# Performance work log

Hardware: AMD Instinct MI355X
Metric: run time of the kernel (lower is better)

## Reference

```python
import jax, jax.numpy as jnp
import numpy as np

VAR0, VAR1 = 0.1, 0.2      # cfg['variance']
THR = 0.5                   # overlap_thresh
NEGPOS_RATIO = 3


def point_form(p):  # center form [P,4] -> corner form
    return jnp.concatenate([p[:, :2] - p[:, 2:] / 2, p[:, :2] + p[:, 2:] / 2], axis=1)


def iou(a, b):  # a [N,4], b [P,4], both corner form -> [N,P]
    lt = jnp.maximum(a[:, None, :2], b[None, :, :2])
    rb = jnp.minimum(a[:, None, 2:], b[None, :, 2:])
    wh = jnp.maximum(rb - lt, 0.0)
    inter = wh[..., 0] * wh[..., 1]
    area_a = (a[:, 2] - a[:, 0]) * (a[:, 3] - a[:, 1])
    area_b = (b[:, 2] - b[:, 0]) * (b[:, 3] - b[:, 1])
    return inter / (area_a[:, None] + area_b[None, :] - inter)


def encode(matched, priors):  # matched corner [P,4], priors center [P,4]
    g_cxcy = ((matched[:, :2] + matched[:, 2:]) / 2 - priors[:, :2]) / (VAR0 * priors[:, 2:])
    g_wh = jnp.log((matched[:, 2:] - matched[:, :2]) / priors[:, 2:]) / VAR1
    return jnp.concatenate([g_cxcy, g_wh], axis=1)


def match_one(truths, labels, priors):
    # truths [N,4] corner, labels [N] int, priors [P,4] center
    ov = iou(truths, point_form(priors))            # [N,P]
    best_prior_idx = jnp.argmax(ov, axis=1)         # [N] best prior per truth
    best_truth_overlap = jnp.max(ov, axis=0)        # [P]
    best_truth_idx = jnp.argmax(ov, axis=0)         # [P]
    # ensure every truth keeps its best prior
    best_truth_overlap = best_truth_overlap.at[best_prior_idx].set(2.0)
    best_truth_idx = best_truth_idx.at[best_prior_idx].set(jnp.arange(truths.shape[0]))
    matched = truths[best_truth_idx]                # [P,4]
    conf = jnp.where(best_truth_overlap < THR, 0, labels[best_truth_idx] + 1)  # bkg=0
    return encode(matched, priors), conf


def multibox_loss(loc_data, conf_data, priors, truths, labels):
    B, P, C = conf_data.shape
    loc_t, conf_t = jax.vmap(lambda t, l: match_one(t, l, priors))(truths, labels)
    loc_t = jax.lax.stop_gradient(loc_t)            # targets are detached
    pos = conf_t > 0                                # [B,P]

    # localization: masked smooth-L1 (beta=1), sum reduction
    d = loc_data - loc_t
    ad = jnp.abs(d)
    sl1 = jnp.where(ad < 1.0, 0.5 * d * d, ad - 0.5)
    loss_l = jnp.sum(sl1 * pos[..., None].astype(sl1.dtype))

    # hard negative mining: per-prior CE proxy, positives zeroed, double argsort rank
    lse = jax.nn.logsumexp(conf_data, axis=2)
    gathered = jnp.take_along_axis(conf_data, conf_t[..., None], axis=2)[..., 0]
    lc = jnp.where(pos, 0.0, lse - gathered)        # [B,P]
    loss_idx = jnp.argsort(-lc, axis=1)
    idx_rank = jnp.argsort(loss_idx, axis=1)
    num_pos = jnp.sum(pos, axis=1)                  # [B]
    num_neg = jnp.minimum(NEGPOS_RATIO * num_pos, P - 1)
    neg = idx_rank < num_neg[:, None]
    sel = pos | neg

    # confidence loss on pos + hard negatives, sum reduction
    logp = jax.nn.log_softmax(conf_data, axis=2)
    ce = -jnp.take_along_axis(logp, conf_t[..., None], axis=2)[..., 0]
    loss_c = jnp.sum(ce * sel.astype(ce.dtype))

    total = jnp.sum(num_pos).astype(loss_l.dtype)
    return loss_l / total, loss_c / total


def setup_inputs() -> dict:
    key = jax.random.key(0)
    kl, kc, kp, kt, ky = jax.random.split(key, 5)
    B, P, C, N = 64, 24564, 21, 16
    loc_data = 0.1 * jax.random.normal(kl, (B, P, 4), dtype=jnp.float32)
    conf_data = jax.random.normal(kc, (B, P, C), dtype=jnp.float32)
    pr = jax.random.uniform(kp, (P, 4), dtype=jnp.float32)
    priors = jnp.concatenate([pr[:, :2] * 0.9 + 0.05, pr[:, 2:] * 0.26 + 0.04], axis=1)
    pts = jax.random.uniform(kt, (B, N, 2, 2), dtype=jnp.float32) * 0.8 + 0.05
    truths = jnp.concatenate([jnp.min(pts, axis=2), jnp.max(pts, axis=2) + 0.02], axis=-1)
    labels = jax.random.randint(ky, (B, N), 0, 20, dtype=jnp.int32)
    return {"loc_data": loc_data, "conf_data": conf_data, "priors": priors,
            "truths": truths, "labels": labels}


def reference(loc_data, conf_data, priors, truths, labels):
    return multibox_loss(loc_data, conf_data, priors, truths, labels)
```

## Files before the change

kernel.cpp:

```cpp
#include <hip/hip_runtime.h>
#include <math.h>

constexpr int Bn = 64;
constexpr int Pn = 24564;
constexpr int Cn = 21;
constexpr int Nn = 16;
constexpr int CH = 12;
constexpr int CHSZ = 2048;
constexpr float VAR0 = 0.1f, VAR1 = 0.2f, THRv = 0.5f;

__device__ __forceinline__ float iou_tp(float tx1, float ty1, float tx2, float ty2,
                                        float px1, float py1, float px2, float py2) {
  float lx = fmaxf(tx1, px1), ly = fmaxf(ty1, py1);
  float rx = fminf(tx2, px2), ry = fminf(ty2, py2);
  float w = fmaxf(rx - lx, 0.f), h = fmaxf(ry - ly, 0.f);
  float inter = w * h;
  float aa = (tx2 - tx1) * (ty2 - ty1);
  float ab = (px2 - px1) * (py2 - py1);
  return inter / (aa + ab - inter);
}

__global__ void best_prior_part(const float* __restrict__ priors,
                                const float* __restrict__ truths,
                                float* __restrict__ pbv, int* __restrict__ pbi) {
  const int c = blockIdx.x;
  const int b = blockIdx.y;
  const int tid = threadIdx.x;
  __shared__ float4 tru[Nn];
  if (tid < Nn) tru[tid] = reinterpret_cast<const float4*>(truths)[b * Nn + tid];
  __syncthreads();

  float bv[Nn];
  int bi[Nn];
#pragma unroll
  for (int n = 0; n < Nn; n++) { bv[n] = -1.0f; bi[n] = 0x7fffffff; }

  const int base = c * CHSZ;
#pragma unroll
  for (int j = 0; j < CHSZ / 256; j++) {
    int p = base + j * 256 + tid;
    if (p < Pn) {
      float4 pr = reinterpret_cast<const float4*>(priors)[p];
      float px1 = pr.x - pr.z * 0.5f, py1 = pr.y - pr.w * 0.5f;
      float px2 = pr.x + pr.z * 0.5f, py2 = pr.y + pr.w * 0.5f;
#pragma unroll
      for (int n = 0; n < Nn; n++) {
        float v = iou_tp(tru[n].x, tru[n].y, tru[n].z, tru[n].w, px1, py1, px2, py2);
        if (v > bv[n]) { bv[n] = v; bi[n] = p; }
      }
    }
  }

  const int lane = tid & 63, wv = tid >> 6;
  __shared__ float swv[4][Nn];
  __shared__ int swi[4][Nn];
#pragma unroll
  for (int n = 0; n < Nn; n++) {
    float v = bv[n]; int i = bi[n];
#pragma unroll
    for (int m = 1; m < 64; m <<= 1) {
      float ov = __shfl_xor(v, m, 64);
      int oi = __shfl_xor(i, m, 64);
      if (ov > v || (ov == v && oi < i)) { v = ov; i = oi; }
    }
    if (lane == 0) { swv[wv][n] = v; swi[wv][n] = i; }
  }
  __syncthreads();
  if (tid < Nn) {
    float v = swv[0][tid]; int i = swi[0][tid];
#pragma unroll
    for (int w = 1; w < 4; w++) {
      float ov = swv[w][tid]; int oi = swi[w][tid];
      if (ov > v || (ov == v && oi < i)) { v = ov; i = oi; }
    }
    pbv[(b * CH + c) * Nn + tid] = v;
    pbi[(b * CH + c) * Nn + tid] = i;
  }
}

__global__ void best_prior_merge(const float* __restrict__ pbv,
                                 const int* __restrict__ pbi,
                                 int* __restrict__ bpi) {
  const int b = blockIdx.x;
  const int n = threadIdx.x;
  if (n < Nn) {
    float v = pbv[(b * CH) * Nn + n];
    int i = pbi[(b * CH) * Nn + n];
#pragma unroll
    for (int c = 1; c < CH; c++) {
      float ov = pbv[(b * CH + c) * Nn + n];
      int oi = pbi[(b * CH + c) * Nn + n];
      if (ov > v || (ov == v && oi < i)) { v = ov; i = oi; }
    }
    bpi[b * Nn + n] = i;
  }
}

__global__ void match_loss_kernel(const float* __restrict__ loc,
                                  const float* __restrict__ conf,
                                  const float* __restrict__ priors,
                                  const float* __restrict__ truths,
                                  const int* __restrict__ labels,
                                  const int* __restrict__ bpi,
                                  float* __restrict__ lc_out,
                                  int* __restrict__ num_pos,
                                  float* __restrict__ acc ) {
  const int b = blockIdx.y;
  const int tid = threadIdx.x;
  const int p = blockIdx.x * blockDim.x + tid;

  __shared__ float4 tru[Nn];
  __shared__ int lab[Nn];
  __shared__ int bp[Nn];
  if (tid < Nn) {
    tru[tid] = reinterpret_cast<const float4*>(truths)[b * Nn + tid];
    lab[tid] = labels[b * Nn + tid];
    bp[tid]  = bpi[b * Nn + tid];
  }
  __syncthreads();

  float my_ll = 0.f, my_cep = 0.f;
  int my_np = 0;

  if (p < Pn) {
    float4 pr = reinterpret_cast<const float4*>(priors)[p];
    float px1 = pr.x - pr.z * 0.5f, py1 = pr.y - pr.w * 0.5f;
    float px2 = pr.x + pr.z * 0.5f, py2 = pr.y + pr.w * 0.5f;

    float best = -1.0f;
    int bidx = 0;
#pragma unroll
    for (int n = 0; n < Nn; n++) {
      float v = iou_tp(tru[n].x, tru[n].y, tru[n].z, tru[n].w, px1, py1, px2, py2);
      if (v > best) { best = v; bidx = n; }
    }
#pragma unroll
    for (int n = 0; n < Nn; n++) {
      if (bp[n] == p) { best = 2.0f; bidx = n; }
    }

    int conf_t = (best < THRv) ? 0 : (lab[bidx] + 1);
    bool pos = conf_t > 0;

    const float* crow = conf + ((size_t)b * Pn + p) * Cn;
    float m = -INFINITY;
#pragma unroll
    for (int c = 0; c < Cn; c++) m = fmaxf(m, crow[c]);
    float s = 0.f;
#pragma unroll
    for (int c = 0; c < Cn; c++) s += __expf(crow[c] - m);
    float lse = m + __logf(s);
    float ce = lse - crow[conf_t];

    lc_out[(size_t)b * Pn + p] = pos ? 0.f : ce;

    if (pos) {
      my_np = 1;
      my_cep = ce;
      float4 t = tru[bidx];
      float gx = ((t.x + t.z) * 0.5f - pr.x) / (VAR0 * pr.z);
      float gy = ((t.y + t.w) * 0.5f - pr.y) / (VAR0 * pr.w);
      float gw = __logf((t.z - t.x) / pr.z) / VAR1;
      float gh = __logf((t.w - t.y) / pr.w) / VAR1;
      const float* lrow = loc + ((size_t)b * Pn + p) * 4;
      float d0 = lrow[0] - gx, d1 = lrow[1] - gy, d2 = lrow[2] - gw, d3 = lrow[3] - gh;
      float a0 = fabsf(d0), a1 = fabsf(d1), a2 = fabsf(d2), a3 = fabsf(d3);
      my_ll  = (a0 < 1.f ? 0.5f * d0 * d0 : a0 - 0.5f);
      my_ll += (a1 < 1.f ? 0.5f * d1 * d1 : a1 - 0.5f);
      my_ll += (a2 < 1.f ? 0.5f * d2 * d2 : a2 - 0.5f);
      my_ll += (a3 < 1.f ? 0.5f * d3 * d3 : a3 - 0.5f);
    }
  }

  __shared__ float sll[256];
  __shared__ float sce[256];
  __shared__ int snp[256];
  sll[tid] = my_ll; sce[tid] = my_cep; snp[tid] = my_np;
  __syncthreads();
  for (int s2 = 128; s2 > 0; s2 >>= 1) {
    if (tid < s2) {
      sll[tid] += sll[tid + s2];
      sce[tid] += sce[tid + s2];
      snp[tid] += snp[tid + s2];
    }
    __syncthreads();
  }
  if (tid == 0) {
    if (sll[0] != 0.f) atomicAdd(&acc[0], sll[0]);
    if (sce[0] != 0.f) atomicAdd(&acc[1], sce[0]);
    if (snp[0] != 0)   atomicAdd(&num_pos[b], snp[0]);
  }
}

__global__ __launch_bounds__(1024) void topk_kernel(const float* __restrict__ lc,
                                                    const int* __restrict__ num_pos,
                                                    float* __restrict__ topk) {
  const int b = blockIdx.x;
  const int tid = threadIdx.x;
  const int wv = tid >> 6, lane = tid & 63;
  const float* row = lc + (size_t)b * Pn;
  const int K = min(3 * num_pos[b], Pn - 1);

  __shared__ unsigned cnt[16][256];
  __shared__ float bsum[16][256];
  __shared__ unsigned mcnt[256];
  __shared__ float msum[256];
  __shared__ unsigned sh_prefix;
  __shared__ int sh_rem;
  __shared__ float sh_sum;
  __shared__ int sh_done;
  if (tid == 0) { sh_prefix = 0u; sh_rem = K; sh_sum = 0.f; sh_done = (K <= 0) ? 1 : 0; }
  __syncthreads();

  for (int pass = 0; pass < 4; pass++) {
    if (sh_done) break;
    const int shift = 24 - pass * 8;
    for (int q = lane; q < 256; q += 64) { cnt[wv][q] = 0u; bsum[wv][q] = 0.f; }
    __syncthreads();
    const unsigned pref = sh_prefix;
    for (int p = tid; p < Pn; p += 1024) {
      float f = row[p];
      unsigned u = __float_as_uint(f) | 0x80000000u;
      bool match = (pass == 0) || ((u >> (32 - 8 * pass)) == pref);
      if (match) {
        unsigned bkt = (u >> shift) & 255u;
        atomicAdd(&cnt[wv][bkt], 1u);
        atomicAdd(&bsum[wv][bkt], f);
      }
    }
    __syncthreads();
    if (tid < 256) {
      unsigned ctot = 0; float stot = 0.f;
#pragma unroll
      for (int w = 0; w < 16; w++) { ctot += cnt[w][tid]; stot += bsum[w][tid]; }
      mcnt[tid] = ctot; msum[tid] = stot;
    }
    __syncthreads();
    if (tid == 0) {
      int rem = sh_rem;
      float ssum = sh_sum;
      unsigned pivot = 0u;
      int done = 0;
      for (int bkt = 255; bkt >= 0; bkt--) {
        unsigned cb = mcnt[bkt];
        if ((int)cb <= rem) {
          ssum += msum[bkt];
          rem -= (int)cb;
          if (rem == 0) { done = 1; break; }
        } else {
          pivot = (unsigned)bkt;
          break;
        }
      }
      if (!done && pass == 3) {
        unsigned key = (sh_prefix << 8) | pivot;
        float f = __uint_as_float(key & 0x7fffffffu);
        ssum += (float)rem * f;
        done = 1;
      }
      sh_prefix = (sh_prefix << 8) | pivot;
      sh_rem = rem;
      sh_sum = ssum;
      sh_done = done;
    }
    __syncthreads();
  }
  if (tid == 0) topk[b] = sh_sum;
}

__global__ void finalize_kernel(const int* __restrict__ num_pos,
                                const float* __restrict__ topk,
                                const float* __restrict__ acc,
                                float* __restrict__ out) {
  if (threadIdx.x == 0 && blockIdx.x == 0) {
    int tot = 0;
    float tk = 0.f;
    for (int b = 0; b < Bn; b++) { tot += num_pos[b]; tk += topk[b]; }
    float ftot = (float)tot;
    out[0] = acc[0] / ftot;
    out[1] = (acc[1] + tk) / ftot;
  }
}

extern "C" void kernel_launch(void* const* d_in, const int* in_sizes, int n_in,
                              void* d_out, int out_size, void* d_ws, size_t ws_size,
                              hipStream_t stream) {
  const float* loc    = (const float*)d_in[0];
  const float* conf   = (const float*)d_in[1];
  const float* priors = (const float*)d_in[2];
  const float* truths = (const float*)d_in[3];
  const int*   labels = (const int*)d_in[4];
  float* out = (float*)d_out;

  float* lc      = (float*)d_ws;
  int*   num_pos = (int*)(lc + (size_t)Bn * Pn);
  float* topk    = (float*)(num_pos + Bn);
  float* acc     = topk + Bn;
  int*   bpi     = (int*)(acc + 2);
  float* pbv     = (float*)(bpi + Bn * Nn);
  int*   pbi     = (int*)(pbv + Bn * CH * Nn);

  size_t zbytes = (size_t)(Bn + Bn + 2 + Bn * Nn) * 4;
  hipMemsetAsync(num_pos, 0, zbytes, stream);

  dim3 gridA(CH, Bn);
  best_prior_part<<<gridA, 256, 0, stream>>>(priors, truths, pbv, pbi);
  best_prior_merge<<<Bn, 64, 0, stream>>>(pbv, pbi, bpi);

  dim3 gridB((Pn + 255) / 256, Bn);
  match_loss_kernel<<<gridB, 256, 0, stream>>>(loc, conf, priors, truths, labels, bpi,
                                               lc, num_pos, acc);

  topk_kernel<<<Bn, 1024, 0, stream>>>(lc, num_pos, topk);

  finalize_kernel<<<1, 64, 0, stream>>>(num_pos, topk, acc, out);
}
```

Before: 503.0 us.

## Stage conf rows in LDS, use wave shuffles for reductions and histogram

The match/loss kernel now copies each wave's contiguous 64x21 conf slice into shared memory with coalesced float4 loads, replacing strided per-thread row reads. Block reductions switch to wave shuffles plus a 4-entry shared combine. The top-k radix histogram replaces per-element LDS atomics with a warp-aggregated leader loop, and finalize uses one wave shuffle reduction. This adds 21 KB of LDS per block, which may limit occupancy, and the aggregation loop can serialize when buckets are diverse.

```diff
diff --git a/kernel.cpp b/kernel.cpp
--- a/kernel.cpp
+++ b/kernel.cpp
@@ -96,19 +96,23 @@
   }
 }
 
-__global__ void match_loss_kernel(const float* __restrict__ loc,
-                                  const float* __restrict__ conf,
-                                  const float* __restrict__ priors,
-                                  const float* __restrict__ truths,
-                                  const int* __restrict__ labels,
-                                  const int* __restrict__ bpi,
-                                  float* __restrict__ lc_out,
-                                  int* __restrict__ num_pos,
-                                  float* __restrict__ acc ) {
+__global__ __launch_bounds__(256) void match_loss_kernel(
+    const float* __restrict__ loc,
+    const float* __restrict__ conf,
+    const float* __restrict__ priors,
+    const float* __restrict__ truths,
+    const int* __restrict__ labels,
+    const int* __restrict__ bpi,
+    float* __restrict__ lc_out,
+    int* __restrict__ num_pos,
+    float* __restrict__ acc ) {
   const int b = blockIdx.y;
   const int tid = threadIdx.x;
-  const int p = blockIdx.x * blockDim.x + tid;
-
+  const int wv = tid >> 6, lane = tid & 63;
+  const int wbase = blockIdx.x * 256 + wv * 64;
+  const int p = wbase + lane;
+
+  __shared__ float sconf[4][64 * 21];
   __shared__ float4 tru[Nn];
   __shared__ int lab[Nn];
   __shared__ int bp[Nn];
@@ -117,6 +121,13 @@
     lab[tid] = labels[b * Nn + tid];
     bp[tid]  = bpi[b * Nn + tid];
   }
+
+  int vrows = Pn - wbase;
+  vrows = vrows > 64 ? 64 : vrows;
+  const int nf4 = (vrows * 21 + 3) >> 2;
+  const float4* gsrc4 = reinterpret_cast<const float4*>(conf + ((size_t)b * Pn + wbase) * 21);
+  float4* dst4 = reinterpret_cast<float4*>(&sconf[wv][0]);
+  for (int i = lane; i < nf4; i += 64) dst4[i] = gsrc4[i];
   __syncthreads();
 
   float my_ll = 0.f, my_cep = 0.f;
@@ -142,13 +153,17 @@
     int conf_t = (best < THRv) ? 0 : (lab[bidx] + 1);
     bool pos = conf_t > 0;
 
-    const float* crow = conf + ((size_t)b * Pn + p) * Cn;
-    float m = -INFINITY;
-#pragma unroll
-    for (int c = 0; c < Cn; c++) m = fmaxf(m, crow[c]);
+    const float* crow = &sconf[wv][lane * 21];
+    float r[Cn];
+#pragma unroll
+    for (int c = 0; c < Cn; c++) r[c] = crow[c];
+
+    float m = r[0];
+#pragma unroll
+    for (int c = 1; c < Cn; c++) m = fmaxf(m, r[c]);
     float s = 0.f;
 #pragma unroll
-    for (int c = 0; c < Cn; c++) s += __expf(crow[c] - m);
+    for (int c = 0; c < Cn; c++) s += __expf(r[c] - m);
     float lse = m + __logf(s);
     float ce = lse - crow[conf_t];
 
@@ -172,23 +187,25 @@
     }
   }
 
-  __shared__ float sll[256];
-  __shared__ float sce[256];
-  __shared__ int snp[256];
-  sll[tid] = my_ll; sce[tid] = my_cep; snp[tid] = my_np;
-  __syncthreads();
-  for (int s2 = 128; s2 > 0; s2 >>= 1) {
-    if (tid < s2) {
-      sll[tid] += sll[tid + s2];
-      sce[tid] += sce[tid + s2];
-      snp[tid] += snp[tid + s2];
-    }
-    __syncthreads();
-  }
+  float ll = my_ll, cep = my_cep;
+  int np = my_np;
+#pragma unroll
+  for (int m2 = 1; m2 < 64; m2 <<= 1) {
+    ll  += __shfl_xor(ll, m2, 64);
+    cep += __shfl_xor(cep, m2, 64);
+    np  += __shfl_xor(np, m2, 64);
+  }
+  __shared__ float sw_ll[4], sw_ce[4];
+  __shared__ int sw_np[4];
+  if (lane == 0) { sw_ll[wv] = ll; sw_ce[wv] = cep; sw_np[wv] = np; }
+  __syncthreads();
   if (tid == 0) {
-    if (sll[0] != 0.f) atomicAdd(&acc[0], sll[0]);
-    if (sce[0] != 0.f) atomicAdd(&acc[1], sce[0]);
-    if (snp[0] != 0)   atomicAdd(&num_pos[b], snp[0]);
+    float tll = sw_ll[0] + sw_ll[1] + sw_ll[2] + sw_ll[3];
+    float tce = sw_ce[0] + sw_ce[1] + sw_ce[2] + sw_ce[3];
+    int tnp = sw_np[0] + sw_np[1] + sw_np[2] + sw_np[3];
+    if (tll != 0.f) atomicAdd(&acc[0], tll);
+    if (tce != 0.f) atomicAdd(&acc[1], tce);
+    if (tnp != 0)   atomicAdd(&num_pos[b], tnp);
   }
 }
 
@@ -212,20 +229,34 @@
   if (tid == 0) { sh_prefix = 0u; sh_rem = K; sh_sum = 0.f; sh_done = (K <= 0) ? 1 : 0; }
   __syncthreads();
 
+  const int iters = (Pn + 1023) >> 10;
   for (int pass = 0; pass < 4; pass++) {
     if (sh_done) break;
     const int shift = 24 - pass * 8;
     for (int q = lane; q < 256; q += 64) { cnt[wv][q] = 0u; bsum[wv][q] = 0.f; }
     __syncthreads();
     const unsigned pref = sh_prefix;
-    for (int p = tid; p < Pn; p += 1024) {
-      float f = row[p];
+    for (int it = 0; it < iters; it++) {
+      int p = it * 1024 + tid;
+      bool inb = p < Pn;
+      float f = inb ? row[p] : 0.f;
       unsigned u = __float_as_uint(f) | 0x80000000u;
-      bool match = (pass == 0) || ((u >> (32 - 8 * pass)) == pref);
-      if (match) {
-        unsigned bkt = (u >> shift) & 255u;
-        atomicAdd(&cnt[wv][bkt], 1u);
-        atomicAdd(&bsum[wv][bkt], f);
+      bool match = inb && ((pass == 0) || ((u >> (32 - 8 * pass)) == pref));
+      unsigned bkt = (u >> shift) & 255u;
+      unsigned long long active = __ballot(match);
+      while (active) {
+        int leader = __ffsll((unsigned long long)active) - 1;
+        unsigned lbkt = (unsigned)__shfl((int)bkt, leader, 64);
+        bool same = match && (bkt == lbkt);
+        float v = same ? f : 0.f;
+#pragma unroll
+        for (int m = 1; m < 64; m <<= 1) v += __shfl_xor(v, m, 64);
+        unsigned long long mask = __ballot(same);
+        if (lane == leader) {
+          cnt[wv][lbkt] += (unsigned)__popcll(mask);
+          bsum[wv][lbkt] += v;
+        }
+        active &= ~mask;
       }
     }
     __syncthreads();
@@ -272,11 +303,16 @@
                                 const float* __restrict__ topk,
                                 const float* __restrict__ acc,
                                 float* __restrict__ out) {
-  if (threadIdx.x == 0 && blockIdx.x == 0) {
-    int tot = 0;
-    float tk = 0.f;
-    for (int b = 0; b < Bn; b++) { tot += num_pos[b]; tk += topk[b]; }
-    float ftot = (float)tot;
+  const int t = threadIdx.x;
+  int np = num_pos[t];
+  float tk = topk[t];
+#pragma unroll
+  for (int m = 1; m < 64; m <<= 1) {
+    np += __shfl_xor(np, m, 64);
+    tk += __shfl_xor(tk, m, 64);
+  }
+  if (t == 0) {
+    float ftot = (float)np;
     out[0] = acc[0] / ftot;
     out[1] = (acc[1] + tk) / ftot;
   }
```

Measured after the change: 911.9 us. +81.3%, slower.
